# Optimization experiments

Hardware: AMD Instinct MI355X
Metric: run time of the kernel (lower is better)

The kernel has to match this reference:

```python
import jax, jax.numpy as jnp
import numpy as np

LOWRES = 256  # low-res input to coefficient tower
GB = 16       # spatial_bins (grid H=W)
LB = 8        # luma_bins (grid depth)
NIN, NOUT = 3, 3


def _conv_s2(x, w, b):
    # 3x3 stride-2 conv, torch padding=1
    y = jax.lax.conv_general_dilated(x, w, (2, 2), ((1, 1), (1, 1)),
                                     dimension_numbers=('NCHW', 'OIHW', 'NCHW'))
    return y + b[None, :, None, None]


def _pw(x, w, b):
    # 1x1 conv as einsum; w: [O, C]
    return jnp.einsum('bchw,oc->bohw', x, w) + b[None, :, None, None]


def _bilateral_slice(grid, guide, image):
    # grid [B,12,L,GH,GW]; guide [B,H,W] in [0,1]; image [B,NIN,H,W]
    B, C, L, GH, GW = grid.shape
    H, W = guide.shape[1], guide.shape[2]
    cx = (jnp.arange(W, dtype=jnp.float32) + 0.5) * (GW / W) - 0.5
    cy = (jnp.arange(H, dtype=jnp.float32) + 0.5) * (GH / H) - 0.5
    cz = guide * L - 0.5
    x0f = jnp.floor(cx); wx = cx - x0f
    y0f = jnp.floor(cy); wy = cy - y0f
    z0f = jnp.floor(cz); wz = cz - z0f
    x0 = x0f.astype(jnp.int32); y0 = y0f.astype(jnp.int32); z0 = z0f.astype(jnp.int32)
    bidx = jnp.arange(B)[:, None, None]
    acc = jnp.zeros((B, H, W, C), jnp.float32)
    for dz in (0, 1):
        zi = jnp.clip(z0 + dz, 0, L - 1)                     # [B,H,W]
        wzz = wz if dz else (1.0 - wz)
        for dy in (0, 1):
            yi = jnp.clip(y0 + dy, 0, GH - 1)[None, :, None]
            wyy = (wy if dy else (1.0 - wy))[None, :, None]
            for dx in (0, 1):
                xi = jnp.clip(x0 + dx, 0, GW - 1)[None, None, :]
                wxx = (wx if dx else (1.0 - wx))[None, None, :]
                g = grid[bidx, :, zi, yi, xi]                # [B,H,W,C]
                acc = acc + (wzz * wyy * wxx)[..., None] * g
    aff = acc.reshape(B, H, W, NOUT, NIN + 1)
    out = jnp.einsum('bhwci,bihw->bchw', aff[..., :NIN], image) \
        + jnp.transpose(aff[..., NIN], (0, 3, 1, 2))
    return out


def reference(image, val, sw0, sb0, sw1, sb1, sw2, sb2, sw3, sb3, spw, spb,
              lw1, lb1, lw2, lb2, lw3, lb3, cw, cb, fw1, fb1, fw2, fb2,
              gw, gb, ccm_w, ccm_b, shifts, slopes, prw, prb):
    B = image.shape[0]
    low = jax.image.resize(image, (B, NIN, LOWRES, LOWRES), 'bilinear', antialias=False)
    # splat tower: 4 stride-2 3x3 convs + final 1x1 (no relu)
    x = jax.nn.relu(_conv_s2(low, sw0, sb0))
    x = jax.nn.relu(_conv_s2(x, sw1, sb1))
    x = jax.nn.relu(_conv_s2(x, sw2, sb2))
    x = jax.nn.relu(_conv_s2(x, sw3, sb3))           # [B,64,16,16]
    splat = _pw(x, spw, spb) + val                   # + conditioning value
    # local path: three 1x1 convs with relu
    loc = jax.nn.relu(_pw(splat, lw1, lb1))
    loc = jax.nn.relu(_pw(loc, lw2, lb2))
    loc = jax.nn.relu(_pw(loc, lw3, lb3))            # [B,64,16,16]
    # condition path: 1x1 stride-2 conv -> adaptive avgpool(4) -> 2 fc layers
    c = jax.nn.relu(_pw(splat[:, :, ::2, ::2], cw, cb))  # [B,4,8,8]
    c = c.reshape(B, 4, 4, 2, 4, 2).mean(axis=(3, 5))    # [B,4,4,4]
    c = c.reshape(B, 64)
    c = jax.nn.relu(c @ fw1.T + fb1)
    c = jax.nn.relu(c @ fw2.T + fb2)                 # [B,64]
    fused = jax.nn.relu(c[:, :, None, None] + loc)
    coeff = _pw(fused, gw, gb)                       # [B,96,16,16]
    # split into LB chunks of 12 along channels, stack at dim 2
    grid = coeff.reshape(B, LB, NOUT * (NIN + 1), GB, GB).transpose(0, 2, 1, 3, 4)
    # guidemap: ccm -> piecewise-linear curve -> projection -> hardtanh [0,1]
    g = _pw(image, ccm_w, ccm_b)                     # [B,3,H,W]
    g = (slopes * jax.nn.relu(g[..., None] - shifts[None])).sum(-1)
    g = _pw(g, prw, prb)[:, 0]                       # [B,H,W]
    guide = jnp.clip(g, 0.0, 1.0)
    return _bilateral_slice(grid, guide, image)


def setup_inputs() -> dict:
    rng = np.random.default_rng(0)
    def rn(shape, fan_in):
        return jnp.asarray(rng.standard_normal(shape).astype(np.float32) * np.sqrt(2.0 / fan_in))
    B, H, W = 4, 1024, 1024
    d = {}
    d['image'] = jnp.asarray(rng.random((B, 3, H, W), dtype=np.float32))
    d['val'] = jnp.asarray(rng.random((B, 1, 1, 1), dtype=np.float32))
    # splat tower 3->8->16->32->64
    chans = [(3, 8), (8, 16), (16, 32), (32, 64)]
    for i, (ci, co) in enumerate(chans):
        d[f'sw{i}'] = rn((co, ci, 3, 3), ci * 9)
        d[f'sb{i}'] = jnp.zeros((co,), jnp.float32)
    d['spw'] = rn((64, 64), 64); d['spb'] = jnp.zeros((64,), jnp.float32)
    d['lw1'] = rn((128, 64), 64); d['lb1'] = jnp.zeros((128,), jnp.float32)
    d['lw2'] = rn((128, 128), 128); d['lb2'] = jnp.zeros((128,), jnp.float32)
    d['lw3'] = rn((64, 128), 128); d['lb3'] = jnp.zeros((64,), jnp.float32)
    d['cw'] = rn((4, 64), 64); d['cb'] = jnp.zeros((4,), jnp.float32)
    d['fw1'] = rn((64, 64), 64); d['fb1'] = jnp.zeros((64,), jnp.float32)
    d['fw2'] = rn((64, 64), 64); d['fb2'] = jnp.zeros((64,), jnp.float32)
    d['gw'] = rn((96, 64), 64); d['gb'] = jnp.zeros((96,), jnp.float32)
    # guide params (mirrors make_guide_params init)
    d['ccm_w'] = jnp.asarray(np.identity(3, dtype=np.float32)
                             + rng.standard_normal((3, 3)).astype(np.float32) * 1e-4)
    d['ccm_b'] = jnp.zeros((3,), jnp.float32)
    shifts = np.linspace(0, 1, 16, endpoint=False, dtype=np.float32)[None, None, None, :]
    d['shifts'] = jnp.asarray(np.tile(shifts, (3, 1, 1, 1)))
    slopes = np.zeros((1, 3, 1, 1, 16), dtype=np.float32); slopes[..., 0] = 1.0
    d['slopes'] = jnp.asarray(slopes)
    d['prw'] = jnp.ones((1, 3), jnp.float32) / 3.0
    d['prb'] = jnp.zeros((1,), jnp.float32)
    return d
```

## Files before the change

### kernel.cpp

```cpp
#include <hip/hip_runtime.h>

#define BATCH 4
#define HH 1024
#define WW 1024

__global__ __launch_bounds__(256) void dsconv0_k(const float* __restrict__ img,
                                                 const float* __restrict__ wgt,
                                                 const float* __restrict__ bias,
                                                 float* __restrict__ out) {
  int blk = blockIdx.x;
  int tx = blk & 15;
  int ty = (blk >> 4) & 15;
  int b = blk >> 8;
  int t = threadIdx.x;

  __shared__ float low[3][17][21];

  int Y0 = ty << 3, X0 = tx << 3;
  int gy0 = 2 * Y0 - 1, gx0 = 2 * X0 - 1;

  for (int i = t; i < 3 * 17 * 17; i += 256) {
    int c = i / 289;
    int rem = i - c * 289;
    int ly = rem / 17;
    int lx = rem - ly * 17;
    int gy = gy0 + ly, gx = gx0 + lx;
    float v = 0.f;
    if (gy >= 0 && gx >= 0) {
      const float* p = img + (size_t)(b * 3 + c) * HH * WW + (4 * gy + 1) * WW + 4 * gx;
      float4 u0 = *(const float4*)p;
      float4 u1 = *(const float4*)(p + WW);
      v = 0.25f * (u0.y + u0.z + u1.y + u1.z);
    }
    low[c][ly][lx] = v;
  }
  __syncthreads();

  int px = t & 63;
  int og = t >> 6;
  int x = px & 7, y = px >> 3;
  float acc[2];
  acc[0] = bias[og * 2];
  acc[1] = bias[og * 2 + 1];
  for (int ci = 0; ci < 3; ++ci) {
#pragma unroll
    for (int ky = 0; ky < 3; ++ky) {
#pragma unroll
      for (int kx = 0; kx < 3; ++kx) {
        float v = low[ci][2 * y + ky][2 * x + kx];
        acc[0] += wgt[(og * 2) * 27 + ci * 9 + ky * 3 + kx] * v;
        acc[1] += wgt[(og * 2 + 1) * 27 + ci * 9 + ky * 3 + kx] * v;
      }
    }
  }
  float* ob = out + (size_t)b * 8 * 128 * 128 + (Y0 + y) * 128 + X0 + x;
  ob[(og * 2) * 128 * 128] = fmaxf(acc[0], 0.f);
  ob[(og * 2 + 1) * 128 * 128] = fmaxf(acc[1], 0.f);
}

template <int CI, int CO, int HI, int P>
__global__ __launch_bounds__(256) void conv_tile_k(const float* __restrict__ in,
                                                   const float* __restrict__ wgt,
                                                   const float* __restrict__ bias,
                                                   float* __restrict__ out) {
  const int HO = HI / 2;
  const int NT = HO / P;
  const int HALO = 2 * P + 1;
  const int RS = 2 * P + 4;
  constexpr int NO = (CO * P * P) / 256;
  int blk = blockIdx.x;
  int tx = blk % NT;
  int ty = (blk / NT) % NT;
  int b = blk / (NT * NT);
  int t = threadIdx.x;

  __shared__ float s[CI][HALO][RS];

  int Y0 = ty * P, X0 = tx * P;
  int gy0 = 2 * Y0 - 1, gx0 = 2 * X0 - 1;

  for (int i = t; i < CI * HALO * HALO; i += 256) {
    int c = i / (HALO * HALO);
    int rem = i - c * (HALO * HALO);
    int ly = rem / HALO;
    int lx = rem - ly * HALO;
    int gy = gy0 + ly, gx = gx0 + lx;
    float v = 0.f;
    if (gy >= 0 && gy < HI && gx >= 0 && gx < HI)
      v = in[((size_t)(b * CI + c) * HI + gy) * HI + gx];
    s[c][ly][lx] = v;
  }
  __syncthreads();

  int px = t % (P * P);
  int og = t / (P * P);
  int x = px % P, y = px / P;
  float acc[NO];
#pragma unroll
  for (int j = 0; j < NO; ++j) acc[j] = bias[og * NO + j];
  for (int ci = 0; ci < CI; ++ci) {
#pragma unroll
    for (int ky = 0; ky < 3; ++ky) {
#pragma unroll
      for (int kx = 0; kx < 3; ++kx) {
        float v = s[ci][2 * y + ky][2 * x + kx];
#pragma unroll
        for (int j = 0; j < NO; ++j)
          acc[j] += wgt[((og * NO + j) * CI + ci) * 9 + ky * 3 + kx] * v;
      }
    }
  }
#pragma unroll
  for (int j = 0; j < NO; ++j)
    out[(size_t)(b * CO + og * NO + j) * HO * HO + (Y0 + y) * HO + X0 + x] =
        fmaxf(acc[j], 0.f);
}

template <int CI, int RELU>
__device__ __forceinline__ void pw4_c64(const float (*__restrict__ X)[4],
                                        float (*__restrict__ Y)[4],
                                        const float* __restrict__ w,
                                        const float* __restrict__ bias,
                                        float badd, int t) {
  int u = t & 3, og = t >> 2;
  float acc = bias[og] + badd;
#pragma unroll 4
  for (int k = 0; k < CI; k += 4) {
    float4 wv = *(const float4*)&w[og * CI + k];
    acc += wv.x * X[k][u] + wv.y * X[k + 1][u] + wv.z * X[k + 2][u] +
           wv.w * X[k + 3][u];
  }
  if (RELU) acc = fmaxf(acc, 0.f);
  Y[og][u] = acc;
}

template <int CI, int RELU>
__device__ __forceinline__ void pw4_c128(const float (*__restrict__ X)[4],
                                         float (*__restrict__ Y)[4],
                                         const float* __restrict__ w,
                                         const float* __restrict__ bias,
                                         int t) {
  int u0 = (t & 1) << 1, og = t >> 1;
  float a0 = bias[og], a1 = a0;
#pragma unroll 4
  for (int k = 0; k < CI; k += 4) {
    float4 wv = *(const float4*)&w[og * CI + k];
    float2 x0 = *(const float2*)&X[k][u0];
    float2 x1 = *(const float2*)&X[k + 1][u0];
    float2 x2 = *(const float2*)&X[k + 2][u0];
    float2 x3v = *(const float2*)&X[k + 3][u0];
    a0 += wv.x * x0.x + wv.y * x1.x + wv.z * x2.x + wv.w * x3v.x;
    a1 += wv.x * x0.y + wv.y * x1.y + wv.z * x2.y + wv.w * x3v.y;
  }
  if (RELU) { a0 = fmaxf(a0, 0.f); a1 = fmaxf(a1, 0.f); }
  Y[og][u0] = a0;
  Y[og][u0 + 1] = a1;
}

__global__ __launch_bounds__(256) void mlp_k(
    const float* __restrict__ x3, const float* __restrict__ spw,
    const float* __restrict__ spb, const float* __restrict__ val,
    const float* __restrict__ lw1, const float* __restrict__ lb1,
    const float* __restrict__ lw2, const float* __restrict__ lb2,
    const float* __restrict__ lw3, const float* __restrict__ lb3,
    const float* __restrict__ cw, const float* __restrict__ cb,
    const float* __restrict__ fw1, const float* __restrict__ fb1,
    const float* __restrict__ fw2, const float* __restrict__ fb2,
    const float* __restrict__ gw, const float* __restrict__ gb,
    float* __restrict__ gridt) {
  int blk = blockIdx.x;
  int b = blk >> 6;
  int p0 = (blk & 63) << 2;
  int t = threadIdx.x;

  __shared__ __align__(16) float A[128][4];
  __shared__ __align__(16) float Bf[128][4];
  __shared__ float effs[4][64];
  __shared__ float ebv[4];
  __shared__ float s8v[4][64];
  __shared__ float scv[64], h1v[64], f2v[64];

  A[t >> 2][t & 3] = x3[((size_t)(b * 64 + (t >> 2))) * 256 + p0 + (t & 3)];
  {
    int ch = t >> 6, k = t & 63;
    float a = 0.f;
#pragma unroll 8
    for (int o = 0; o < 64; ++o) a += cw[ch * 64 + o] * spw[o * 64 + k];
    effs[ch][k] = a;
    if (k == 0) {
      float a2 = 0.f;
      float vb = val[b];
#pragma unroll 8
      for (int o = 0; o < 64; ++o) a2 += cw[ch * 64 + o] * (spb[o] + vb);
      ebv[ch] = cb[ch] + a2;
    }
  }
  __syncthreads();
  {
    int ch = t >> 6, i = t & 63;
    int p = ((i >> 3) << 5) + ((i & 7) << 1);
    float a = ebv[ch];
#pragma unroll 8
    for (int k = 0; k < 64; ++k)
      a += effs[ch][k] * x3[((size_t)(b * 64 + k)) * 256 + p];
    s8v[ch][i] = fmaxf(a, 0.f);
  }
  __syncthreads();
  if (t < 64) {
    int ch = t >> 4, q = t & 15;
    int py = q >> 2, qx = q & 3;
    int i0 = (py * 2) * 8 + qx * 2;
    scv[t] = 0.25f * (s8v[ch][i0] + s8v[ch][i0 + 1] + s8v[ch][i0 + 8] +
                      s8v[ch][i0 + 9]);
  }
  __syncthreads();

  if (t < 64) {
    float a = fb1[t];
#pragma unroll 8
    for (int k = 0; k < 64; ++k) a += fw1[t * 64 + k] * scv[k];
    h1v[t] = fmaxf(a, 0.f);
  }
  pw4_c64<64, 0>(A, Bf, spw, spb, val[b], t);
  __syncthreads();
  if (t < 64) {
    float a = fb2[t];
#pragma unroll 8
    for (int k = 0; k < 64; ++k) a += fw2[t * 64 + k] * h1v[k];
    f2v[t] = fmaxf(a, 0.f);
  }
  pw4_c128<64, 1>(Bf, A, lw1, lb1, t);
  __syncthreads();
  pw4_c128<128, 1>(A, Bf, lw2, lb2, t);
  __syncthreads();
  pw4_c64<128, 1>(Bf, A, lw3, lb3, 0.f, t);
  __syncthreads();

  {
    int u0 = (t & 1) << 1, og = t >> 1;
    if (og < 96) {
      float a0 = gb[og], a1 = a0;
#pragma unroll 4
      for (int k = 0; k < 64; k += 4) {
        float4 cc4 = *(const float4*)&f2v[k];
        float2 x0 = *(const float2*)&A[k][u0];
        float2 x1 = *(const float2*)&A[k + 1][u0];
        float2 x2 = *(const float2*)&A[k + 2][u0];
        float2 x3v = *(const float2*)&A[k + 3][u0];
        x0.x = fmaxf(x0.x + cc4.x, 0.f); x0.y = fmaxf(x0.y + cc4.x, 0.f);
        x1.x = fmaxf(x1.x + cc4.y, 0.f); x1.y = fmaxf(x1.y + cc4.y, 0.f);
        x2.x = fmaxf(x2.x + cc4.z, 0.f); x2.y = fmaxf(x2.y + cc4.z, 0.f);
        x3v.x = fmaxf(x3v.x + cc4.w, 0.f); x3v.y = fmaxf(x3v.y + cc4.w, 0.f);
        float4 wv = *(const float4*)&gw[og * 64 + k];
        a0 += wv.x * x0.x + wv.y * x1.x + wv.z * x2.x + wv.w * x3v.x;
        a1 += wv.x * x0.y + wv.y * x1.y + wv.z * x2.y + wv.w * x3v.y;
      }
      int l = og / 12, cc = og - l * 12;
      gridt[(size_t)(((b * 8 + l) << 8) + p0 + u0) * 12 + cc] = a0;
      gridt[(size_t)(((b * 8 + l) << 8) + p0 + u0 + 1) * 12 + cc] = a1;
    }
  }
}

#define ZST 200
__global__ __launch_bounds__(256, 6) void slice_k(
    const float* __restrict__ img, const float* __restrict__ gridt,
    const float* __restrict__ ccm_w, const float* __restrict__ ccm_b,
    const float* __restrict__ shifts, const float* __restrict__ slopes,
    const float* __restrict__ prw, const float* __restrict__ prb,
    float* __restrict__ out) {
  int blk = blockIdx.x;
  int b = blk >> 10;
  int h = blk & 1023;
  int t = threadIdx.x;

  __shared__ float sg[8 * ZST];
  __shared__ float2 lut[3][16];

  float cy = (h + 0.5f) * 0.015625f - 0.5f;
  float y0f = floorf(cy);
  float wy = cy - y0f;
  int y0 = (int)y0f;
  int yi0 = min(max(y0, 0), 15), yi1 = min(max(y0 + 1, 0), 15);

  if (t < 48) {
    int c = t >> 4, k = t & 15;
    float cs = 0.f, cbv = 0.f;
    for (int i = 0; i <= k; ++i) {
      float s = slopes[c * 16 + i];
      cs += s;
      cbv += s * shifts[c * 16 + i];
    }
    lut[c][k] = make_float2(cs, cbv);
  }

  for (int i = t; i < 384; i += 256) {
    int z = i / 48;
    int e = i - z * 48;
    const float4* s0 =
        (const float4*)(gridt + (size_t)(((b * 8 + z) << 8) + (yi0 << 4)) * 12);
    const float4* s1 =
        (const float4*)(gridt + (size_t)(((b * 8 + z) << 8) + (yi1 << 4)) * 12);
    float4 a = s0[e], c = s1[e];
    float4 v = make_float4(a.x + wy * (c.x - a.x), a.y + wy * (c.y - a.y),
                           a.z + wy * (c.z - a.z), a.w + wy * (c.w - a.w));
    *((float4*)(sg + z * ZST) + e) = v;
  }
  __syncthreads();

  int pp = (h << 10) + (t << 2);
  const float* ib = img + (size_t)b * 3 * HH * WW;
  float4 R4 = *(const float4*)(ib + pp);
  float4 G4 = *(const float4*)(ib + HH * WW + pp);
  float4 B4 = *(const float4*)(ib + 2 * HH * WW + pp);
  float r_[4] = {R4.x, R4.y, R4.z, R4.w};
  float g_[4] = {G4.x, G4.y, G4.z, G4.w};
  float b_[4] = {B4.x, B4.y, B4.z, B4.w};

  float m0 = ccm_w[0], m1 = ccm_w[1], m2 = ccm_w[2];
  float m3 = ccm_w[3], m4 = ccm_w[4], m5 = ccm_w[5];
  float m6 = ccm_w[6], m7 = ccm_w[7], m8 = ccm_w[8];
  float c0 = ccm_b[0], c1 = ccm_b[1], c2 = ccm_b[2];
  float p0 = prw[0], p1 = prw[1], p2 = prw[2], pb = prb[0];

  float base0 = shifts[0], base1 = shifts[16], base2 = shifts[32];
  float inv0 = 1.0f / (shifts[1] - base0);
  float inv1 = 1.0f / (shifts[17] - base1);
  float inv2 = 1.0f / (shifts[33] - base2);

  float ro[4], go[4], bo[4];
#pragma unroll
  for (int j = 0; j < 4; ++j) {
    float r = r_[j], g = g_[j], bl = b_[j];
    float v0 = c0 + m0 * r + m1 * g + m2 * bl;
    float v1 = c1 + m3 * r + m4 * g + m5 * bl;
    float v2 = c2 + m6 * r + m7 * g + m8 * bl;

    float tv0 = fmaxf(v0, base0);
    float tv1 = fmaxf(v1, base1);
    float tv2 = fmaxf(v2, base2);
    int j0 = min((int)((tv0 - base0) * inv0), 15);
    int j1 = min((int)((tv1 - base1) * inv1), 15);
    int j2 = min((int)((tv2 - base2) * inv2), 15);
    float2 e0 = lut[0][j0];
    float2 e1 = lut[1][j1];
    float2 e2 = lut[2][j2];
    float f0 = e0.x * tv0 - e0.y;
    float f1 = e1.x * tv1 - e1.y;
    float f2 = e2.x * tv2 - e2.y;

    float gg = pb + p0 * f0 + p1 * f1 + p2 * f2;
    float guide = fminf(fmaxf(gg, 0.f), 1.f);

    int w = (t << 2) + j;
    float cx = (w + 0.5f) * 0.015625f - 0.5f;
    float x0f = floorf(cx);
    float wx = cx - x0f;
    int x0i = (int)x0f;
    int xi0 = min(max(x0i, 0), 15), xi1 = min(max(x0i + 1, 0), 15);

    float cz = guide * 8.0f - 0.5f;
    float z0f = floorf(cz);
    float wz = cz - z0f;
    int z0i = (int)z0f;
    int zi0 = min(max(z0i, 0), 7), zi1 = min(max(z0i + 1, 0), 7);

    int oz0 = zi0 * ZST, oz1 = zi1 * ZST;
    int ox0 = xi0 * 12, ox1 = xi1 * 12;
    float wz1 = wz, wz0 = 1.f - wz;
    float wx1 = wx, wx0 = 1.f - wx;

    float rr = 0.f, gg2 = 0.f, bb2 = 0.f;
#pragma unroll
    for (int dz = 0; dz < 2; ++dz) {
      int oz = dz ? oz1 : oz0;
      float wzz = dz ? wz1 : wz0;
#pragma unroll
      for (int dx = 0; dx < 2; ++dx) {
        int ox = dx ? ox1 : ox0;
        float wgt = wzz * (dx ? wx1 : wx0);
        const float* gp = sg + oz + ox;
        float4 a0 = *(const float4*)gp;
        float4 a1 = *(const float4*)(gp + 4);
        float4 a2 = *(const float4*)(gp + 8);
        rr  += wgt * (a0.x * r + a0.y * g + a0.z * bl + a0.w);
        gg2 += wgt * (a1.x * r + a1.y * g + a1.z * bl + a1.w);
        bb2 += wgt * (a2.x * r + a2.y * g + a2.z * bl + a2.w);
      }
    }
    ro[j] = rr;
    go[j] = gg2;
    bo[j] = bb2;
  }
  float* ob = out + (size_t)b * 3 * HH * WW;
  *(float4*)(ob + pp) = make_float4(ro[0], ro[1], ro[2], ro[3]);
  *(float4*)(ob + HH * WW + pp) = make_float4(go[0], go[1], go[2], go[3]);
  *(float4*)(ob + 2 * HH * WW + pp) = make_float4(bo[0], bo[1], bo[2], bo[3]);
}

extern "C" void kernel_launch(void* const* d_in, const int* in_sizes, int n_in,
                              void* d_out, int out_size, void* d_ws, size_t ws_size,
                              hipStream_t stream) {
  const float* image = (const float*)d_in[0];
  const float* val   = (const float*)d_in[1];
  const float* sw0 = (const float*)d_in[2];  const float* sb0 = (const float*)d_in[3];
  const float* sw1 = (const float*)d_in[4];  const float* sb1 = (const float*)d_in[5];
  const float* sw2 = (const float*)d_in[6];  const float* sb2 = (const float*)d_in[7];
  const float* sw3 = (const float*)d_in[8];  const float* sb3 = (const float*)d_in[9];
  const float* spw = (const float*)d_in[10]; const float* spb = (const float*)d_in[11];
  const float* lw1 = (const float*)d_in[12]; const float* lb1 = (const float*)d_in[13];
  const float* lw2 = (const float*)d_in[14]; const float* lb2 = (const float*)d_in[15];
  const float* lw3 = (const float*)d_in[16]; const float* lb3 = (const float*)d_in[17];
  const float* cw  = (const float*)d_in[18]; const float* cb  = (const float*)d_in[19];
  const float* fw1 = (const float*)d_in[20]; const float* fb1 = (const float*)d_in[21];
  const float* fw2 = (const float*)d_in[22]; const float* fb2 = (const float*)d_in[23];
  const float* gw  = (const float*)d_in[24]; const float* gb  = (const float*)d_in[25];
  const float* ccm_w = (const float*)d_in[26]; const float* ccm_b = (const float*)d_in[27];
  const float* shifts = (const float*)d_in[28]; const float* slopes = (const float*)d_in[29];
  const float* prw = (const float*)d_in[30]; const float* prb = (const float*)d_in[31];
  float* out = (float*)d_out;

  float* ws    = (float*)d_ws;
  float* x0    = ws;
  float* x1    = x0 + 524288;
  float* x2    = x1 + 262144;
  float* x3    = x2 + 131072;
  float* gridt = x3 + 65536 + 256;

  dsconv0_k<<<1024, 256, 0, stream>>>(image, sw0, sb0, x0);
  conv_tile_k<8, 16, 128, 4><<<1024, 256, 0, stream>>>(x0, sw1, sb1, x1);
  conv_tile_k<16, 32, 64, 4><<<256, 256, 0, stream>>>(x1, sw2, sb2, x2);
  conv_tile_k<32, 64, 32, 2><<<256, 256, 0, stream>>>(x2, sw3, sb3, x3);
  mlp_k<<<256, 256, 0, stream>>>(x3, spw, spb, val, lw1, lb1, lw2, lb2, lw3, lb3,
                                 cw, cb, fw1, fb1, fw2, fb2, gw, gb, gridt);
  slice_k<<<4096, 256, 0, stream>>>(image, gridt, ccm_w, ccm_b, shifts, slopes,
                                    prw, prb, out);
}
```

Measured before the change: 223.2 us.

## Fuse downsample+conv0 with conv1 into one kernel using halo recompute

Merges the first two stride-2 conv layers into one kernel. Each block loads a larger low-res halo, computes the conv0 outputs it needs into shared memory, and then runs conv1 directly, writing x1. This removes one launch and the global write and read of the x0 intermediate. In exchange it recomputes overlapping conv0 halo values and reads more of the input image per output tile.

```diff
diff --git a/kernel.cpp b/kernel.cpp
--- a/kernel.cpp
+++ b/kernel.cpp
@@ -4,27 +4,31 @@
 #define HH 1024
 #define WW 1024
 
-__global__ __launch_bounds__(256) void dsconv0_k(const float* __restrict__ img,
-                                                 const float* __restrict__ wgt,
-                                                 const float* __restrict__ bias,
-                                                 float* __restrict__ out) {
+__global__ __launch_bounds__(256) void ds01_k(const float* __restrict__ img,
+                                              const float* __restrict__ w0,
+                                              const float* __restrict__ b0,
+                                              const float* __restrict__ w1,
+                                              const float* __restrict__ b1,
+                                              float* __restrict__ out) {
   int blk = blockIdx.x;
   int tx = blk & 15;
   int ty = (blk >> 4) & 15;
   int b = blk >> 8;
   int t = threadIdx.x;
 
-  __shared__ float low[3][17][21];
-
-  int Y0 = ty << 3, X0 = tx << 3;
+  __shared__ float low[3][19][21];
+  __shared__ float x0s[8][9][12];
+
+  int Y0 = ty << 2, X0 = tx << 2;
   int gy0 = 2 * Y0 - 1, gx0 = 2 * X0 - 1;
-
-  for (int i = t; i < 3 * 17 * 17; i += 256) {
-    int c = i / 289;
-    int rem = i - c * 289;
-    int ly = rem / 17;
-    int lx = rem - ly * 17;
-    int gy = gy0 + ly, gx = gx0 + lx;
+  int ly0 = 2 * gy0 - 1, lx0 = 2 * gx0 - 1;
+
+  for (int i = t; i < 3 * 19 * 19; i += 256) {
+    int c = i / 361;
+    int rem = i - c * 361;
+    int ly = rem / 19;
+    int lx = rem - ly * 19;
+    int gy = ly0 + ly, gx = lx0 + lx;
     float v = 0.f;
     if (gy >= 0 && gx >= 0) {
       const float* p = img + (size_t)(b * 3 + c) * HH * WW + (4 * gy + 1) * WW + 4 * gx;
@@ -36,26 +40,44 @@
   }
   __syncthreads();
 
-  int px = t & 63;
-  int og = t >> 6;
-  int x = px & 7, y = px >> 3;
-  float acc[2];
-  acc[0] = bias[og * 2];
-  acc[1] = bias[og * 2 + 1];
-  for (int ci = 0; ci < 3; ++ci) {
-#pragma unroll
-    for (int ky = 0; ky < 3; ++ky) {
-#pragma unroll
-      for (int kx = 0; kx < 3; ++kx) {
-        float v = low[ci][2 * y + ky][2 * x + kx];
-        acc[0] += wgt[(og * 2) * 27 + ci * 9 + ky * 3 + kx] * v;
-        acc[1] += wgt[(og * 2 + 1) * 27 + ci * 9 + ky * 3 + kx] * v;
-      }
-    }
-  }
-  float* ob = out + (size_t)b * 8 * 128 * 128 + (Y0 + y) * 128 + X0 + x;
-  ob[(og * 2) * 128 * 128] = fmaxf(acc[0], 0.f);
-  ob[(og * 2 + 1) * 128 * 128] = fmaxf(acc[1], 0.f);
+  for (int i = t; i < 8 * 81; i += 256) {
+    int ch = i / 81;
+    int pos = i - ch * 81;
+    int py = pos / 9, px = pos - py * 9;
+    int gy = gy0 + py, gx = gx0 + px;
+    float v = 0.f;
+    if (gy >= 0 && gx >= 0) {
+      float a = b0[ch];
+#pragma unroll
+      for (int ci = 0; ci < 3; ++ci)
+#pragma unroll
+        for (int ky = 0; ky < 3; ++ky)
+#pragma unroll
+          for (int kx = 0; kx < 3; ++kx)
+            a += low[ci][2 * py + ky][2 * px + kx] *
+                 w0[ch * 27 + ci * 9 + ky * 3 + kx];
+      v = fmaxf(a, 0.f);
+    }
+    x0s[ch][py][px] = v;
+  }
+  __syncthreads();
+
+  {
+    int oc = t >> 4;
+    int pos = t & 15;
+    int y = pos >> 2, x = pos & 3;
+    float a = b1[oc];
+#pragma unroll
+    for (int ci = 0; ci < 8; ++ci)
+#pragma unroll
+      for (int ky = 0; ky < 3; ++ky)
+#pragma unroll
+        for (int kx = 0; kx < 3; ++kx)
+          a += x0s[ci][2 * y + ky][2 * x + kx] *
+               w1[(oc * 8 + ci) * 9 + ky * 3 + kx];
+    out[(size_t)(b * 16 + oc) * 64 * 64 + (Y0 + y) * 64 + X0 + x] =
+        fmaxf(a, 0.f);
+  }
 }
 
 template <int CI, int CO, int HI, int P>
@@ -427,8 +449,7 @@
   float* x3    = x2 + 131072;
   float* gridt = x3 + 65536 + 256;
 
-  dsconv0_k<<<1024, 256, 0, stream>>>(image, sw0, sb0, x0);
-  conv_tile_k<8, 16, 128, 4><<<1024, 256, 0, stream>>>(x0, sw1, sb1, x1);
+  ds01_k<<<1024, 256, 0, stream>>>(image, sw0, sb0, sw1, sb1, x1);
   conv_tile_k<16, 32, 64, 4><<<256, 256, 0, stream>>>(x1, sw2, sb2, x2);
   conv_tile_k<32, 64, 32, 2><<<256, 256, 0, stream>>>(x2, sw3, sb3, x3);
   mlp_k<<<256, 256, 0, stream>>>(x3, spw, spb, val, lw1, lb1, lw2, lb2, lw3, lb3,
```

After: 223.1 us. About the same (-0.0%).
